# Performance work log

Hardware: AMD Instinct MI355X
Metric: run time of the kernel (lower is better)

## Reference

```python
import jax, jax.numpy as jnp
import numpy as np

BETA = 0.25  # commitment loss weight


def setup_inputs() -> dict:
    key = jax.random.key(0)
    k1, k2 = jax.random.split(key)
    x = jax.random.normal(k1, (64, 64, 64, 64), dtype=jnp.float32)
    # embeddings: [embedding_dim=64, num_embeddings=512], random_uniform init in [-0.05, 0.05]
    embeddings = jax.random.uniform(k2, (64, 512), dtype=jnp.float32, minval=-0.05, maxval=0.05)
    return {"x": x, "embeddings": embeddings}


def reference(x, embeddings):
    d = embeddings.shape[0]
    flat = x.reshape(-1, d)                                   # [N, D]
    # squared L2 distances to each code: ||z||^2 + ||e||^2 - 2 z.e
    sim = flat @ embeddings                                   # [N, K]
    dist = (jnp.sum(flat * flat, axis=1, keepdims=True)
            + jnp.sum(embeddings * embeddings, axis=0)
            - 2.0 * sim)                                      # [N, K]
    idx = jnp.argmin(dist, axis=1)                            # [N]
    # gather nearest code (equivalent to one_hot @ embeddings.T)
    quantized = jnp.take(embeddings.T, idx, axis=0).reshape(x.shape)
    commitment_loss = jnp.mean((jax.lax.stop_gradient(quantized) - x) ** 2)
    codebook_loss = jnp.mean((quantized - jax.lax.stop_gradient(x)) ** 2)
    loss = BETA * commitment_loss + codebook_loss
    # straight-through estimator
    quantized_st = x + jax.lax.stop_gradient(quantized - x)
    return quantized_st, loss
```

## Files before the change

kernel.cpp:

```cpp
#include <hip/hip_runtime.h>


#define NROWS 262144
#define D 64
#define K 512
#define MARGIN 0.09f
#define INF32 3.4e38f

#define WS_ET 0
#define WS_E2 131072
#define WS_EBT 133120
#define WS_PARTIALS 198656

typedef __attribute__((ext_vector_type(8))) short bf16x8;
typedef __attribute__((ext_vector_type(4))) float f32x4;

__device__ inline unsigned short f2bf(float f) {
    unsigned u = __float_as_uint(f);
    u += 0x7fffu + ((u >> 16) & 1u);
    return (unsigned short)(u >> 16);
}
__device__ inline unsigned pack_bf2(float lo, float hi) {
    unsigned ulo = __float_as_uint(lo); ulo += 0x7fffu + ((ulo >> 16) & 1u);
    unsigned uhi = __float_as_uint(hi); uhi += 0x7fffu + ((uhi >> 16) & 1u);
    return (ulo >> 16) | (uhi & 0xffff0000u);
}
__device__ inline bf16x8 pack8(float4 p, float4 q) {
    union { unsigned u[4]; bf16x8 v; } r;
    r.u[0] = pack_bf2(p.x, p.y); r.u[1] = pack_bf2(p.z, p.w);
    r.u[2] = pack_bf2(q.x, q.y); r.u[3] = pack_bf2(q.z, q.w);
    return r.v;
}

__global__ void __launch_bounds__(64) vq_prep(const float* __restrict__ emb, char* ws) {
    float* e2 = (float*)(ws + WS_E2);
    float* et = (float*)(ws + WS_ET);
    unsigned short* ebT = (unsigned short*)(ws + WS_EBT);
    int k = blockIdx.x * 64 + threadIdx.x;
    float v0 = emb[k];
    et[k * D] = v0;
    ebT[k * D] = f2bf(v0);
    float s = __fmul_rn(v0, v0);
    for (int d = 1; d < D; ++d) {
        float v = emb[d * K + k];
        et[k * D + d] = v;
        ebT[k * D + d] = f2bf(v);
        s = __fadd_rn(s, __fmul_rn(v, v));
    }
    e2[k] = s;
}

__device__ __noinline__ unsigned long long exact_pack(
        const float* __restrict__ x, const float* __restrict__ et,
        const float* __restrict__ e2f, int row, int k) {
    const float* xr = x + (size_t)row * D;
    float r0 = __fmul_rn(xr[0], xr[0]), r1 = __fmul_rn(xr[1], xr[1]);
    float r2 = __fmul_rn(xr[2], xr[2]), r3 = __fmul_rn(xr[3], xr[3]);
    float r4 = __fmul_rn(xr[4], xr[4]), r5 = __fmul_rn(xr[5], xr[5]);
    float r6 = __fmul_rn(xr[6], xr[6]), r7 = __fmul_rn(xr[7], xr[7]);
    for (int i = 8; i < 64; i += 8) {
        r0 = __fadd_rn(r0, __fmul_rn(xr[i],     xr[i]));
        r1 = __fadd_rn(r1, __fmul_rn(xr[i + 1], xr[i + 1]));
        r2 = __fadd_rn(r2, __fmul_rn(xr[i + 2], xr[i + 2]));
        r3 = __fadd_rn(r3, __fmul_rn(xr[i + 3], xr[i + 3]));
        r4 = __fadd_rn(r4, __fmul_rn(xr[i + 4], xr[i + 4]));
        r5 = __fadd_rn(r5, __fmul_rn(xr[i + 5], xr[i + 5]));
        r6 = __fadd_rn(r6, __fmul_rn(xr[i + 6], xr[i + 6]));
        r7 = __fadd_rn(r7, __fmul_rn(xr[i + 7], xr[i + 7]));
    }
    float z2 = __fadd_rn(__fadd_rn(__fadd_rn(r0, r1), __fadd_rn(r2, r3)),
                         __fadd_rn(__fadd_rn(r4, r5), __fadd_rn(r6, r7)));
    const float* ep = et + (size_t)k * D;
    float a = 0.f;
    for (int d = 0; d < D; ++d) a = fmaf(xr[d], ep[d], a);
    float dist = __fsub_rn(__fadd_rn(z2, e2f[k]), __fmul_rn(2.0f, a));
    return ((unsigned long long)__float_as_uint(dist) << 32) | (unsigned)k;
}

__global__ void __launch_bounds__(64)
__attribute__((amdgpu_waves_per_eu(4, 4)))
vq_fused(const float* __restrict__ x, float* __restrict__ out,
         char* __restrict__ ws) {
    const float* et  = (const float*)(ws + WS_ET);
    const float* e2f = (const float*)(ws + WS_E2);
    const unsigned short* ebT = (const unsigned short*)(ws + WS_EBT);
    double* partials = (double*)(ws + WS_PARTIALS);

    __shared__ float le2[512];
    __shared__ unsigned long long lgmin[64];
    __shared__ unsigned cl[1024];
    __shared__ int ccnt;
    __shared__ int ovf;

    const int lane = threadIdx.x;
    const int c15 = lane & 15;
    const int g = lane >> 4;
    const int kofs = g * 8;
    const int gr4 = g * 4;
    const int bswz = (blockIdx.x & 7) * 512 + (blockIdx.x >> 3);
    const int rowBase = bswz * 64;

    lgmin[lane] = 0xFFFFFFFFFFFFFFFFULL;
    if (lane == 0) { ccnt = 0; ovf = 0; }
#pragma unroll
    for (int i = 0; i < 8; ++i) le2[i * 64 + lane] = e2f[i * 64 + lane];

    bf16x8 aA0, aA1, aB0, aB1, aC0, aC1, aD0, aD1;
#define LOADA(RT, A0, A1) { \
    const float* xp = x + ((size_t)(rowBase + (RT) * 16 + c15)) * D + kofs; \
    float4 p0 = *(const float4*)xp; \
    float4 p1 = *(const float4*)(xp + 4); \
    float4 p2 = *(const float4*)(xp + 32); \
    float4 p3 = *(const float4*)(xp + 36); \
    A0 = pack8(p0, p1); A1 = pack8(p2, p3); }
    LOADA(0, aA0, aA1) LOADA(1, aB0, aB1) LOADA(2, aC0, aC1) LOADA(3, aD0, aD1)
#undef LOADA

    __syncthreads();

    float m00 = INF32, m01 = INF32, m02 = INF32, m03 = INF32;
    float m10 = INF32, m11 = INF32, m12 = INF32, m13 = INF32;
    float m20 = INF32, m21 = INF32, m22 = INF32, m23 = INF32;
    float m30 = INF32, m31 = INF32, m32 = INF32, m33 = INF32;

    const unsigned short* bbase = ebT + ((size_t)c15 << 6) + kofs;

#define SW1(A0, A1, M0, M1, M2, M3) { \
    f32x4 acc = {0.f, 0.f, 0.f, 0.f}; \
    acc = __builtin_amdgcn_mfma_f32_16x16x32_bf16(A0, bb0, acc, 0, 0, 0); \
    acc = __builtin_amdgcn_mfma_f32_16x16x32_bf16(A1, bb1, acc, 0, 0, 0); \
    M0 = fminf(M0, fmaf(-2.0f, acc[0], e2c)); \
    M1 = fminf(M1, fmaf(-2.0f, acc[1], e2c)); \
    M2 = fminf(M2, fmaf(-2.0f, acc[2], e2c)); \
    M3 = fminf(M3, fmaf(-2.0f, acc[3], e2c)); }

    {
        bf16x8 bb0 = *(const bf16x8*)bbase;
        bf16x8 bb1 = *(const bf16x8*)(bbase + 32);
        for (int j = 0; j < 32; ++j) {
            const unsigned short* np = bbase + (((j + 1) & 31) << 10);
            bf16x8 nb0 = *(const bf16x8*)np;
            bf16x8 nb1 = *(const bf16x8*)(np + 32);
            float e2c = le2[j * 16 + c15];
            SW1(aA0, aA1, m00, m01, m02, m03)
            SW1(aB0, aB1, m10, m11, m12, m13)
            SW1(aC0, aC1, m20, m21, m22, m23)
            SW1(aD0, aD1, m30, m31, m32, m33)
            bb0 = nb0; bb1 = nb1;
        }
    }
#undef SW1

#define RED(v) v = fminf(v, __shfl_xor(v, 1)); v = fminf(v, __shfl_xor(v, 2)); \
               v = fminf(v, __shfl_xor(v, 4)); v = fminf(v, __shfl_xor(v, 8)); \
               v += MARGIN;
    RED(m00) RED(m01) RED(m02) RED(m03)
    RED(m10) RED(m11) RED(m12) RED(m13)
    RED(m20) RED(m21) RED(m22) RED(m23)
    RED(m30) RED(m31) RED(m32) RED(m33)
#undef RED

#define PUSH(RT, R) { int idx = atomicAdd(&ccnt, 1); \
    if (idx < 1024) cl[idx] = \
        ((unsigned)((RT) * 16 + gr4 + (R)) << 9) | (unsigned)kkl; \
    else ovf = 1; }

#define SW2(RT, A0, A1, M0, M1, M2, M3) { \
    f32x4 acc = {0.f, 0.f, 0.f, 0.f}; \
    acc = __builtin_amdgcn_mfma_f32_16x16x32_bf16(A0, bb0, acc, 0, 0, 0); \
    acc = __builtin_amdgcn_mfma_f32_16x16x32_bf16(A1, bb1, acc, 0, 0, 0); \
    if (fmaf(-2.0f, acc[0], e2c) <= M0) PUSH(RT, 0) \
    if (fmaf(-2.0f, acc[1], e2c) <= M1) PUSH(RT, 1) \
    if (fmaf(-2.0f, acc[2], e2c) <= M2) PUSH(RT, 2) \
    if (fmaf(-2.0f, acc[3], e2c) <= M3) PUSH(RT, 3) }

    {
        bf16x8 bb0 = *(const bf16x8*)bbase;
        bf16x8 bb1 = *(const bf16x8*)(bbase + 32);
        for (int j = 0; j < 32; ++j) {
            const unsigned short* np = bbase + (((j + 1) & 31) << 10);
            bf16x8 nb0 = *(const bf16x8*)np;
            bf16x8 nb1 = *(const bf16x8*)(np + 32);
            const int kkl = j * 16 + c15;
            float e2c = le2[kkl];
            SW2(0, aA0, aA1, m00, m01, m02, m03)
            SW2(1, aB0, aB1, m10, m11, m12, m13)
            SW2(2, aC0, aC1, m20, m21, m22, m23)
            SW2(3, aD0, aD1, m30, m31, m32, m33)
            bb0 = nb0; bb1 = nb1;
        }
    }
#undef SW2
#undef PUSH

    __syncthreads();
    const int cnt = (ccnt < 1024) ? ccnt : 1024;
    for (int i = lane; i < cnt; i += 64) {
        unsigned e = cl[i];
        int rowLocal = (int)(e >> 9);
        int k = (int)(e & 0x1ffu);
        atomicMin(&lgmin[rowLocal], exact_pack(x, et, e2f, rowBase + rowLocal, k));
    }
    if (ovf) {
        for (int p = lane; p < 64 * 512; p += 64)
            atomicMin(&lgmin[p >> 9],
                      exact_pack(x, et, e2f, rowBase + (p >> 9), p & 0x1ff));
    }
    __syncthreads();

    const int row = rowBase + lane;
    const int kb = (int)(lgmin[lane] & 0xFFFFFFFFULL);
    const float4* cq = (const float4*)(et + (size_t)kb * D);
    const float4* xr = (const float4*)(x + (size_t)row * D);
    float4* outr = (float4*)(out + (size_t)row * D);
    double rs = 0.0;
#define OUTQ(G) { \
        float4 e4 = cq[G]; float4 xv = xr[G]; float4 o; \
        float d0 = __fsub_rn(e4.x, xv.x); \
        float d1 = __fsub_rn(e4.y, xv.y); \
        float d2 = __fsub_rn(e4.z, xv.z); \
        float d3 = __fsub_rn(e4.w, xv.w); \
        o.x = __fadd_rn(xv.x, d0); \
        o.y = __fadd_rn(xv.y, d1); \
        o.z = __fadd_rn(xv.z, d2); \
        o.w = __fadd_rn(xv.w, d3); \
        outr[G] = o; \
        rs += (double)__fmul_rn(d0, d0) + (double)__fmul_rn(d1, d1) + \
              (double)__fmul_rn(d2, d2) + (double)__fmul_rn(d3, d3); }
    OUTQ(0) OUTQ(1) OUTQ(2) OUTQ(3) OUTQ(4) OUTQ(5) OUTQ(6) OUTQ(7)
    OUTQ(8) OUTQ(9) OUTQ(10) OUTQ(11) OUTQ(12) OUTQ(13) OUTQ(14) OUTQ(15)
#undef OUTQ

#pragma unroll
    for (int off = 32; off > 0; off >>= 1) rs += __shfl_down(rs, off);
    if (lane == 0) partials[bswz] = rs;
}

__global__ void __launch_bounds__(256) vq_finalize(float* __restrict__ out, char* ws) {
    const double* partials = (const double*)(ws + WS_PARTIALS);
    __shared__ double red[256];
    double s = 0.0;
#pragma unroll
    for (int i = 0; i < 16; ++i) s += partials[threadIdx.x + 256 * i];
    red[threadIdx.x] = s;
    __syncthreads();
    for (int st = 128; st > 0; st >>= 1) {
        if (threadIdx.x < st) red[threadIdx.x] += red[threadIdx.x + st];
        __syncthreads();
    }
    if (threadIdx.x == 0) {
        out[16777216] = (float)(1.25 * red[0] / 16777216.0);
    }
}

extern "C" void kernel_launch(void* const* d_in, const int* in_sizes, int n_in,
                              void* d_out, int out_size, void* d_ws, size_t ws_size,
                              hipStream_t stream) {
    const float* x   = (const float*)d_in[0];
    const float* emb = (const float*)d_in[1];
    float* out = (float*)d_out;
    char* ws = (char*)d_ws;

    vq_prep<<<8, 64, 0, stream>>>(emb, ws);
    vq_fused<<<NROWS / 64, 64, 0, stream>>>(x, out, ws);
    vq_finalize<<<1, 256, 0, stream>>>(out, ws);
}
```

Baseline: 170.3 us.

## Use 4-wave blocks of 128 rows with 32 rows per wave

Restructures the fused VQ kernel from a single 64-row wave per block into 256-thread blocks covering 128 rows, with each wave handling 32 rows (two MFMA row tiles instead of four). The shared candidate list, the exact rescoring and the output pass are now spread across all 256 threads, with two threads per row writing the output, and the per-block loss partial is reduced through shared memory. The intent is to raise parallelism and occupancy by lowering per-wave register pressure and sharing the e2 table load. In exchange, each wave now streams the full codebook for only half as many rows, and block-level barriers and a tree reduction are added.

```diff
diff --git a/kernel.cpp b/kernel.cpp
--- a/kernel.cpp
+++ b/kernel.cpp
@@ -77,8 +77,7 @@
     return ((unsigned long long)__float_as_uint(dist) << 32) | (unsigned)k;
 }
 
-__global__ void __launch_bounds__(64)
-__attribute__((amdgpu_waves_per_eu(4, 4)))
+__global__ void __launch_bounds__(256)
 vq_fused(const float* __restrict__ x, float* __restrict__ out,
          char* __restrict__ ws) {
     const float* et  = (const float*)(ws + WS_ET);
@@ -87,25 +86,28 @@
     double* partials = (double*)(ws + WS_PARTIALS);
 
     __shared__ float le2[512];
-    __shared__ unsigned long long lgmin[64];
-    __shared__ unsigned cl[1024];
+    __shared__ unsigned long long lgmin[128];
+    __shared__ unsigned cl[2048];
+    __shared__ double red[256];
     __shared__ int ccnt;
     __shared__ int ovf;
 
-    const int lane = threadIdx.x;
+    const int tid = threadIdx.x;
+    const int wv = tid >> 6, lane = tid & 63;
     const int c15 = lane & 15;
     const int g = lane >> 4;
     const int kofs = g * 8;
     const int gr4 = g * 4;
-    const int bswz = (blockIdx.x & 7) * 512 + (blockIdx.x >> 3);
-    const int rowBase = bswz * 64;
-
-    lgmin[lane] = 0xFFFFFFFFFFFFFFFFULL;
-    if (lane == 0) { ccnt = 0; ovf = 0; }
-#pragma unroll
-    for (int i = 0; i < 8; ++i) le2[i * 64 + lane] = e2f[i * 64 + lane];
-
-    bf16x8 aA0, aA1, aB0, aB1, aC0, aC1, aD0, aD1;
+    const int bswz = ((int)blockIdx.x & 7) * 256 + ((int)blockIdx.x >> 3);
+    const int blockRow0 = bswz * 128;
+    const int rowBase = blockRow0 + wv * 32;
+
+    if (tid < 128) lgmin[tid] = 0xFFFFFFFFFFFFFFFFULL;
+    if (tid == 0) { ccnt = 0; ovf = 0; }
+    le2[tid] = e2f[tid];
+    le2[tid + 256] = e2f[tid + 256];
+
+    bf16x8 aA0, aA1, aB0, aB1;
 #define LOADA(RT, A0, A1) { \
     const float* xp = x + ((size_t)(rowBase + (RT) * 16 + c15)) * D + kofs; \
     float4 p0 = *(const float4*)xp; \
@@ -113,15 +115,13 @@
     float4 p2 = *(const float4*)(xp + 32); \
     float4 p3 = *(const float4*)(xp + 36); \
     A0 = pack8(p0, p1); A1 = pack8(p2, p3); }
-    LOADA(0, aA0, aA1) LOADA(1, aB0, aB1) LOADA(2, aC0, aC1) LOADA(3, aD0, aD1)
+    LOADA(0, aA0, aA1) LOADA(1, aB0, aB1)
 #undef LOADA
 
     __syncthreads();
 
     float m00 = INF32, m01 = INF32, m02 = INF32, m03 = INF32;
     float m10 = INF32, m11 = INF32, m12 = INF32, m13 = INF32;
-    float m20 = INF32, m21 = INF32, m22 = INF32, m23 = INF32;
-    float m30 = INF32, m31 = INF32, m32 = INF32, m33 = INF32;
 
     const unsigned short* bbase = ebT + ((size_t)c15 << 6) + kofs;
 
@@ -144,8 +144,6 @@
             float e2c = le2[j * 16 + c15];
             SW1(aA0, aA1, m00, m01, m02, m03)
             SW1(aB0, aB1, m10, m11, m12, m13)
-            SW1(aC0, aC1, m20, m21, m22, m23)
-            SW1(aD0, aD1, m30, m31, m32, m33)
             bb0 = nb0; bb1 = nb1;
         }
     }
@@ -156,13 +154,11 @@
                v += MARGIN;
     RED(m00) RED(m01) RED(m02) RED(m03)
     RED(m10) RED(m11) RED(m12) RED(m13)
-    RED(m20) RED(m21) RED(m22) RED(m23)
-    RED(m30) RED(m31) RED(m32) RED(m33)
 #undef RED
 
 #define PUSH(RT, R) { int idx = atomicAdd(&ccnt, 1); \
-    if (idx < 1024) cl[idx] = \
-        ((unsigned)((RT) * 16 + gr4 + (R)) << 9) | (unsigned)kkl; \
+    if (idx < 2048) cl[idx] = \
+        ((unsigned)(wv * 32 + (RT) * 16 + gr4 + (R)) << 9) | (unsigned)kkl; \
     else ovf = 1; }
 
 #define SW2(RT, A0, A1, M0, M1, M2, M3) { \
@@ -185,8 +181,6 @@
             float e2c = le2[kkl];
             SW2(0, aA0, aA1, m00, m01, m02, m03)
             SW2(1, aB0, aB1, m10, m11, m12, m13)
-            SW2(2, aC0, aC1, m20, m21, m22, m23)
-            SW2(3, aD0, aD1, m30, m31, m32, m33)
             bb0 = nb0; bb1 = nb1;
         }
     }
@@ -194,25 +188,27 @@
 #undef PUSH
 
     __syncthreads();
-    const int cnt = (ccnt < 1024) ? ccnt : 1024;
-    for (int i = lane; i < cnt; i += 64) {
+    const int cnt = (ccnt < 2048) ? ccnt : 2048;
+    for (int i = tid; i < cnt; i += 256) {
         unsigned e = cl[i];
         int rowLocal = (int)(e >> 9);
         int k = (int)(e & 0x1ffu);
-        atomicMin(&lgmin[rowLocal], exact_pack(x, et, e2f, rowBase + rowLocal, k));
+        atomicMin(&lgmin[rowLocal], exact_pack(x, et, e2f, blockRow0 + rowLocal, k));
     }
     if (ovf) {
-        for (int p = lane; p < 64 * 512; p += 64)
+        for (int p = tid; p < 128 * 512; p += 256)
             atomicMin(&lgmin[p >> 9],
-                      exact_pack(x, et, e2f, rowBase + (p >> 9), p & 0x1ff));
-    }
-    __syncthreads();
-
-    const int row = rowBase + lane;
-    const int kb = (int)(lgmin[lane] & 0xFFFFFFFFULL);
-    const float4* cq = (const float4*)(et + (size_t)kb * D);
-    const float4* xr = (const float4*)(x + (size_t)row * D);
-    float4* outr = (float4*)(out + (size_t)row * D);
+                      exact_pack(x, et, e2f, blockRow0 + (p >> 9), p & 0x1ff));
+    }
+    __syncthreads();
+
+    const int rowL = tid >> 1;
+    const int half = tid & 1;
+    const int row = blockRow0 + rowL;
+    const int kb = (int)(lgmin[rowL] & 0xFFFFFFFFULL);
+    const float4* cq = (const float4*)(et + (size_t)kb * D) + half * 8;
+    const float4* xr = (const float4*)(x + (size_t)row * D) + half * 8;
+    float4* outr = (float4*)(out + (size_t)row * D) + half * 8;
     double rs = 0.0;
 #define OUTQ(G) { \
         float4 e4 = cq[G]; float4 xv = xr[G]; float4 o; \
@@ -228,12 +224,15 @@
         rs += (double)__fmul_rn(d0, d0) + (double)__fmul_rn(d1, d1) + \
               (double)__fmul_rn(d2, d2) + (double)__fmul_rn(d3, d3); }
     OUTQ(0) OUTQ(1) OUTQ(2) OUTQ(3) OUTQ(4) OUTQ(5) OUTQ(6) OUTQ(7)
-    OUTQ(8) OUTQ(9) OUTQ(10) OUTQ(11) OUTQ(12) OUTQ(13) OUTQ(14) OUTQ(15)
 #undef OUTQ
 
-#pragma unroll
-    for (int off = 32; off > 0; off >>= 1) rs += __shfl_down(rs, off);
-    if (lane == 0) partials[bswz] = rs;
+    red[tid] = rs;
+    __syncthreads();
+    for (int s = 128; s > 0; s >>= 1) {
+        if (tid < s) red[tid] += red[tid + s];
+        __syncthreads();
+    }
+    if (tid == 0) partials[bswz] = red[0];
 }
 
 __global__ void __launch_bounds__(256) vq_finalize(float* __restrict__ out, char* ws) {
@@ -241,7 +240,7 @@
     __shared__ double red[256];
     double s = 0.0;
 #pragma unroll
-    for (int i = 0; i < 16; ++i) s += partials[threadIdx.x + 256 * i];
+    for (int i = 0; i < 8; ++i) s += partials[threadIdx.x + 256 * i];
     red[threadIdx.x] = s;
     __syncthreads();
     for (int st = 128; st > 0; st >>= 1) {
@@ -262,6 +261,6 @@
     char* ws = (char*)d_ws;
 
     vq_prep<<<8, 64, 0, stream>>>(emb, ws);
-    vq_fused<<<NROWS / 64, 64, 0, stream>>>(x, out, ws);
+    vq_fused<<<NROWS / 128, 256, 0, stream>>>(x, out, ws);
     vq_finalize<<<1, 256, 0, stream>>>(out, ws);
 }
```

After: 236.5 us. 1.39x slower.

## Stage half of A fragments in LDS and drop fixed waves-per-EU hint

Applied to the files above, without the earlier changes.

Keeps the bf16 A fragments for only two of the four row tiles in registers and stores the other two in shared memory (duplicated into two buffers indexed by loop parity), reloading them every iteration of both MFMA sweeps. The fixed waves_per_eu(4,4) attribute is removed and the candidate list is halved to 512 entries. The aim is to cut register pressure so the compiler can run more waves per SIMD, trading that for extra LDS reads in the inner loops and a higher chance of hitting the slow overflow fallback.

```diff
diff --git a/kernel.cpp b/kernel.cpp
--- a/kernel.cpp
+++ b/kernel.cpp
@@ -78,7 +78,6 @@
 }
 
 __global__ void __launch_bounds__(64)
-__attribute__((amdgpu_waves_per_eu(4, 4)))
 vq_fused(const float* __restrict__ x, float* __restrict__ out,
          char* __restrict__ ws) {
     const float* et  = (const float*)(ws + WS_ET);
@@ -87,8 +86,9 @@
     double* partials = (double*)(ws + WS_PARTIALS);
 
     __shared__ float le2[512];
+    __shared__ uint4 aS[2][2][2][64];
     __shared__ unsigned long long lgmin[64];
-    __shared__ unsigned cl[1024];
+    __shared__ unsigned cl[512];
     __shared__ int ccnt;
     __shared__ int ovf;
 
@@ -97,7 +97,7 @@
     const int g = lane >> 4;
     const int kofs = g * 8;
     const int gr4 = g * 4;
-    const int bswz = (blockIdx.x & 7) * 512 + (blockIdx.x >> 3);
+    const int bswz = ((int)blockIdx.x & 7) * 512 + ((int)blockIdx.x >> 3);
     const int rowBase = bswz * 64;
 
     lgmin[lane] = 0xFFFFFFFFFFFFFFFFULL;
@@ -105,7 +105,7 @@
 #pragma unroll
     for (int i = 0; i < 8; ++i) le2[i * 64 + lane] = e2f[i * 64 + lane];
 
-    bf16x8 aA0, aA1, aB0, aB1, aC0, aC1, aD0, aD1;
+    bf16x8 aA0, aA1, aB0, aB1;
 #define LOADA(RT, A0, A1) { \
     const float* xp = x + ((size_t)(rowBase + (RT) * 16 + c15)) * D + kofs; \
     float4 p0 = *(const float4*)xp; \
@@ -113,8 +113,21 @@
     float4 p2 = *(const float4*)(xp + 32); \
     float4 p3 = *(const float4*)(xp + 36); \
     A0 = pack8(p0, p1); A1 = pack8(p2, p3); }
-    LOADA(0, aA0, aA1) LOADA(1, aB0, aB1) LOADA(2, aC0, aC1) LOADA(3, aD0, aD1)
+    LOADA(0, aA0, aA1) LOADA(1, aB0, aB1)
 #undef LOADA
+
+#define STOREA(RT, IDX) { \
+    const float* xp = x + ((size_t)(rowBase + (RT) * 16 + c15)) * D + kofs; \
+    float4 p0 = *(const float4*)xp; \
+    float4 p1 = *(const float4*)(xp + 4); \
+    float4 p2 = *(const float4*)(xp + 32); \
+    float4 p3 = *(const float4*)(xp + 36); \
+    union { bf16x8 v; uint4 u; } c0, c1; \
+    c0.v = pack8(p0, p1); c1.v = pack8(p2, p3); \
+    aS[0][IDX][0][lane] = c0.u; aS[0][IDX][1][lane] = c1.u; \
+    aS[1][IDX][0][lane] = c0.u; aS[1][IDX][1][lane] = c1.u; }
+    STOREA(2, 0) STOREA(3, 1)
+#undef STOREA
 
     __syncthreads();
 
@@ -125,7 +138,7 @@
 
     const unsigned short* bbase = ebT + ((size_t)c15 << 6) + kofs;
 
-#define SW1(A0, A1, M0, M1, M2, M3) { \
+#define SWM(A0, A1, M0, M1, M2, M3) { \
     f32x4 acc = {0.f, 0.f, 0.f, 0.f}; \
     acc = __builtin_amdgcn_mfma_f32_16x16x32_bf16(A0, bb0, acc, 0, 0, 0); \
     acc = __builtin_amdgcn_mfma_f32_16x16x32_bf16(A1, bb1, acc, 0, 0, 0); \
@@ -142,14 +155,16 @@
             bf16x8 nb0 = *(const bf16x8*)np;
             bf16x8 nb1 = *(const bf16x8*)(np + 32);
             float e2c = le2[j * 16 + c15];
-            SW1(aA0, aA1, m00, m01, m02, m03)
-            SW1(aB0, aB1, m10, m11, m12, m13)
-            SW1(aC0, aC1, m20, m21, m22, m23)
-            SW1(aD0, aD1, m30, m31, m32, m33)
+            union { uint4 u; bf16x8 v; } t20, t21, t30, t31;
+            t20.u = aS[j & 1][0][0][lane]; t21.u = aS[j & 1][0][1][lane];
+            t30.u = aS[j & 1][1][0][lane]; t31.u = aS[j & 1][1][1][lane];
+            SWM(aA0, aA1, m00, m01, m02, m03)
+            SWM(aB0, aB1, m10, m11, m12, m13)
+            SWM(t20.v, t21.v, m20, m21, m22, m23)
+            SWM(t30.v, t31.v, m30, m31, m32, m33)
             bb0 = nb0; bb1 = nb1;
         }
     }
-#undef SW1
 
 #define RED(v) v = fminf(v, __shfl_xor(v, 1)); v = fminf(v, __shfl_xor(v, 2)); \
                v = fminf(v, __shfl_xor(v, 4)); v = fminf(v, __shfl_xor(v, 8)); \
@@ -161,11 +176,11 @@
 #undef RED
 
 #define PUSH(RT, R) { int idx = atomicAdd(&ccnt, 1); \
-    if (idx < 1024) cl[idx] = \
+    if (idx < 512) cl[idx] = \
         ((unsigned)((RT) * 16 + gr4 + (R)) << 9) | (unsigned)kkl; \
     else ovf = 1; }
 
-#define SW2(RT, A0, A1, M0, M1, M2, M3) { \
+#define SWC(RT, A0, A1, M0, M1, M2, M3) { \
     f32x4 acc = {0.f, 0.f, 0.f, 0.f}; \
     acc = __builtin_amdgcn_mfma_f32_16x16x32_bf16(A0, bb0, acc, 0, 0, 0); \
     acc = __builtin_amdgcn_mfma_f32_16x16x32_bf16(A1, bb1, acc, 0, 0, 0); \
@@ -183,18 +198,22 @@
             bf16x8 nb1 = *(const bf16x8*)(np + 32);
             const int kkl = j * 16 + c15;
             float e2c = le2[kkl];
-            SW2(0, aA0, aA1, m00, m01, m02, m03)
-            SW2(1, aB0, aB1, m10, m11, m12, m13)
-            SW2(2, aC0, aC1, m20, m21, m22, m23)
-            SW2(3, aD0, aD1, m30, m31, m32, m33)
+            union { uint4 u; bf16x8 v; } t20, t21, t30, t31;
+            t20.u = aS[j & 1][0][0][lane]; t21.u = aS[j & 1][0][1][lane];
+            t30.u = aS[j & 1][1][0][lane]; t31.u = aS[j & 1][1][1][lane];
+            SWC(0, aA0, aA1, m00, m01, m02, m03)
+            SWC(1, aB0, aB1, m10, m11, m12, m13)
+            SWC(2, t20.v, t21.v, m20, m21, m22, m23)
+            SWC(3, t30.v, t31.v, m30, m31, m32, m33)
             bb0 = nb0; bb1 = nb1;
         }
     }
-#undef SW2
+#undef SWC
 #undef PUSH
-
-    __syncthreads();
-    const int cnt = (ccnt < 1024) ? ccnt : 1024;
+#undef SWM
+
+    __syncthreads();
+    const int cnt = (ccnt < 512) ? ccnt : 512;
     for (int i = lane; i < cnt; i += 64) {
         unsigned e = cl[i];
         int rowLocal = (int)(e >> 9);
```

New measurement: 208.4 us. 22.3% more time.
